# Kernel optimization log

Measured on AMD Instinct MI355X. Metric: run time of the kernel, lower is better.

## Reference

```python
import jax, jax.numpy as jnp
import numpy as np


def setup_inputs() -> dict:
    key = jax.random.key(0)
    k1, k2 = jax.random.split(key)
    B, N, M, D = 4, 8192, 8192, 3
    inp = jax.random.normal(k1, (B, N, D), dtype=jnp.float32)
    pnt = jax.random.normal(k2, (B, M, D), dtype=jnp.float32)
    return {"input": inp, "point": pnt}


def reference(input, point):
    # Per-query nearest-neighbor squared distance:
    # out[b, n] = min_m || input[b, n] - point[b, m] ||^2
    # Use ||a||^2 + ||b||^2 - 2 a.b to avoid materializing [B, N, M, D].
    sq_in = jnp.sum(input * input, axis=-1)          # [B, N]
    sq_pt = jnp.sum(point * point, axis=-1)          # [B, M]
    cross = jnp.einsum('bnd,bmd->bnm', input, point) # [B, N, M]
    d2 = sq_in[:, :, None] + sq_pt[:, None, :] - 2.0 * cross
    d2 = jnp.maximum(d2, 0.0)  # numerical guard
    return jnp.min(d2, axis=-1)  # [B, N]
```

## Files before the change

kernel.cpp:

```cpp
#include <hip/hip_runtime.h>
#include <hip/hip_bf16.h>

constexpr int B = 4;
constexpr int N = 8192;
constexpr int M = 8192;

constexpr int QPW     = 64;
constexpr int WAVES   = 4;
constexpr int QB      = QPW * WAVES;
constexpr int QTILES  = N / QB;
constexpr int PCHUNKS = 16;
constexpr int CHUNK   = M / PCHUNKS;
constexpr int PTILES  = CHUNK / 32;

typedef __bf16 bf16x8 __attribute__((ext_vector_type(8)));
typedef float  f32x16 __attribute__((ext_vector_type(16)));

union FragU { uint4 u; bf16x8 b; };

__device__ __host__ inline unsigned f2bf(float x) {
    unsigned u = __float_as_uint(x);
    return (u + 0x7FFFu + ((u >> 16) & 1u)) >> 16;
}
__device__ inline float bf2f(unsigned b) { return __uint_as_float(b << 16); }
__device__ inline unsigned pk(unsigned lo, unsigned hi) { return lo | (hi << 16); }


__global__ __launch_bounds__(256) void prep_kernel(const float* __restrict__ point,
                                                   uint4* __restrict__ wtab,
                                                   unsigned int* __restrict__ out) {
    int i = blockIdx.x * 256 + threadIdx.x;
    if (i >= B * M) return;
    const float p0 = point[3 * i + 0];
    const float p1 = point[3 * i + 1];
    const float p2 = point[3 * i + 2];
    const float v0 = -2.0f * p0, v1 = -2.0f * p1, v2 = -2.0f * p2;
    const unsigned h0 = f2bf(v0), l0 = f2bf(v0 - bf2f(h0));
    const unsigned h1 = f2bf(v1), l1 = f2bf(v1 - bf2f(h1));
    const unsigned h2 = f2bf(v2), l2 = f2bf(v2 - bf2f(h2));
    const float s = fmaf(p0, p0, fmaf(p1, p1, p2 * p2));
    const unsigned sh = f2bf(s), sl = f2bf(s - bf2f(sh));
    uint4 f0, f1;
    f0.x = pk(h0, h0); f0.y = pk(l0, l0); f0.z = pk(h1, h1); f0.w = pk(l1, l1);
    f1.x = pk(h2, h2); f1.y = pk(l2, l2); f1.z = pk(sh, sl); f1.w = 0;
    wtab[2 * i + 0] = f0;
    wtab[2 * i + 1] = f1;
    out[i] = 0x7F7F7F7Fu;
}

__device__ inline FragU make_bfrag(const float* __restrict__ input,
                                   int b, int q, int h, float& sq_a) {
    const float* a = input + ((size_t)b * N + q) * 3;
    const float a0 = a[0], a1 = a[1], a2 = a[2];
    sq_a = fmaf(a0, a0, fmaf(a1, a1, a2 * a2));
    const unsigned ah0 = f2bf(a0), al0 = f2bf(a0 - bf2f(ah0));
    const unsigned ah1 = f2bf(a1), al1 = f2bf(a1 - bf2f(ah1));
    const unsigned ah2 = f2bf(a2), al2 = f2bf(a2 - bf2f(ah2));
    FragU bq;
    const unsigned dA = h ? pk(ah2, al2) : pk(ah0, al0);
    const unsigned dB = h ? 0x3F803F80u  : pk(ah1, al1);
    bq.u.x = dA;
    bq.u.y = dA;
    bq.u.z = dB;
    bq.u.w = h ? 0u : dB;
    return bq;
}

__global__ __launch_bounds__(256, 3) void main_kernel(const float* __restrict__ input,
                                                      const uint4* __restrict__ wtab,
                                                      unsigned int* __restrict__ out) {
    const int bid    = blockIdx.x;
    const int pchunk = bid % PCHUNKS;
    const int qtile  = (bid / PCHUNKS) % QTILES;
    const int b      = bid / (PCHUNKS * QTILES);
    const int tid    = threadIdx.x;
    const int wave   = tid >> 6;
    const int lane   = tid & 63;
    const int col    = lane & 31;
    const int h      = lane >> 5;

    const int q0 = qtile * QB + wave * QPW + col;
    const int q1 = q0 + 32;
    float sq_a0, sq_a1;
    const FragU b0 = make_bfrag(input, b, q0, h, sq_a0);
    const FragU b1 = make_bfrag(input, b, q1, h, sq_a1);

    const uint4* __restrict__ wp =
        wtab + ((size_t)b * M + (size_t)pchunk * CHUNK) * 2;

    f32x16 cz, rmin0, rmin1;
#pragma unroll
    for (int i = 0; i < 16; ++i) { cz[i] = 0.0f; rmin0[i] = 1e30f; rmin1[i] = 1e30f; }

    for (int t = 0; t < PTILES; t += 2) {
        FragU fa0, fa1;
        fa0.u = wp[((t * 32 + col) << 1) + h];
        fa1.u = wp[(((t + 1) * 32 + col) << 1) + h];
        f32x16 acc00 = __builtin_amdgcn_mfma_f32_32x32x16_bf16(fa0.b, b0.b, cz, 0, 0, 0);
        f32x16 acc01 = __builtin_amdgcn_mfma_f32_32x32x16_bf16(fa0.b, b1.b, cz, 0, 0, 0);
        f32x16 acc10 = __builtin_amdgcn_mfma_f32_32x32x16_bf16(fa1.b, b0.b, cz, 0, 0, 0);
        f32x16 acc11 = __builtin_amdgcn_mfma_f32_32x32x16_bf16(fa1.b, b1.b, cz, 0, 0, 0);
#pragma unroll
        for (int i = 0; i < 16; ++i) {
            rmin0[i] = fminf(rmin0[i], fminf(acc00[i], acc10[i]));
            rmin1[i] = fminf(rmin1[i], fminf(acc01[i], acc11[i]));
        }
    }

    float m0 = rmin0[0], m1 = rmin1[0];
#pragma unroll
    for (int i = 1; i < 16; ++i) { m0 = fminf(m0, rmin0[i]); m1 = fminf(m1, rmin1[i]); }
    m0 = fminf(m0, __shfl_xor(m0, 32, 64));
    m1 = fminf(m1, __shfl_xor(m1, 32, 64));

    if (lane < 32) {
        atomicMin(&out[(size_t)b * N + q0], __float_as_uint(fmaxf(m0 + sq_a0, 0.0f)));
        atomicMin(&out[(size_t)b * N + q1], __float_as_uint(fmaxf(m1 + sq_a1, 0.0f)));
    }
}

extern "C" void kernel_launch(void* const* d_in, const int* in_sizes, int n_in,
                              void* d_out, int out_size, void* d_ws, size_t ws_size,
                              hipStream_t stream) {
    const float* input = (const float*)d_in[0];
    const float* point = (const float*)d_in[1];
    unsigned int* out  = (unsigned int*)d_out;

    uint4* wtab = (uint4*)d_ws;

    const int prep_grid = (B * M + 255) / 256;
    const int main_grid = B * QTILES * PCHUNKS;

    prep_kernel<<<prep_grid, 256, 0, stream>>>(point, wtab, out);
    main_kernel<<<main_grid, 256, 0, stream>>>(input, wtab, out);
}
```

Before: 66.52 us.

## Fuse point packing into main kernel via shared-memory tile, memset output

Removes the separate prep kernel and its global workspace table. Each block now loads its chunk of raw points, packs them into bf16 hi/lo fragments in LDS, and has the MFMA loop read from LDS instead of global memory. Output initialisation moves to a hipMemsetAsync. The packing work is repeated once per query tile (QTILES times per chunk), and the LDS footprint is 16KB per block, which may limit occupancy.

```diff
diff --git a/kernel.cpp b/kernel.cpp
--- a/kernel.cpp
+++ b/kernel.cpp
@@ -18,7 +18,7 @@
 
 union FragU { uint4 u; bf16x8 b; };
 
-__device__ __host__ inline unsigned f2bf(float x) {
+__device__ inline unsigned f2bf(float x) {
     unsigned u = __float_as_uint(x);
     return (u + 0x7FFFu + ((u >> 16) & 1u)) >> 16;
 }
@@ -26,26 +26,16 @@
 __device__ inline unsigned pk(unsigned lo, unsigned hi) { return lo | (hi << 16); }
 
 
-__global__ __launch_bounds__(256) void prep_kernel(const float* __restrict__ point,
-                                                   uint4* __restrict__ wtab,
-                                                   unsigned int* __restrict__ out) {
-    int i = blockIdx.x * 256 + threadIdx.x;
-    if (i >= B * M) return;
-    const float p0 = point[3 * i + 0];
-    const float p1 = point[3 * i + 1];
-    const float p2 = point[3 * i + 2];
+__device__ inline void pack_point(float p0, float p1, float p2,
+                                  uint4& f0, uint4& f1) {
     const float v0 = -2.0f * p0, v1 = -2.0f * p1, v2 = -2.0f * p2;
     const unsigned h0 = f2bf(v0), l0 = f2bf(v0 - bf2f(h0));
     const unsigned h1 = f2bf(v1), l1 = f2bf(v1 - bf2f(h1));
     const unsigned h2 = f2bf(v2), l2 = f2bf(v2 - bf2f(h2));
     const float s = fmaf(p0, p0, fmaf(p1, p1, p2 * p2));
     const unsigned sh = f2bf(s), sl = f2bf(s - bf2f(sh));
-    uint4 f0, f1;
     f0.x = pk(h0, h0); f0.y = pk(l0, l0); f0.z = pk(h1, h1); f0.w = pk(l1, l1);
     f1.x = pk(h2, h2); f1.y = pk(l2, l2); f1.z = pk(sh, sl); f1.w = 0;
-    wtab[2 * i + 0] = f0;
-    wtab[2 * i + 1] = f1;
-    out[i] = 0x7F7F7F7Fu;
 }
 
 __device__ inline FragU make_bfrag(const float* __restrict__ input,
@@ -67,7 +57,7 @@
 }
 
 __global__ __launch_bounds__(256, 3) void main_kernel(const float* __restrict__ input,
-                                                      const uint4* __restrict__ wtab,
+                                                      const float* __restrict__ point,
                                                       unsigned int* __restrict__ out) {
     const int bid    = blockIdx.x;
     const int pchunk = bid % PCHUNKS;
@@ -79,14 +69,32 @@
     const int col    = lane & 31;
     const int h      = lane >> 5;
 
+    __shared__ uint4 tile[2][CHUNK];
+
+    {
+        const float* pp = point + ((size_t)b * M + (size_t)pchunk * CHUNK) * 3;
+        const float2* pp2 = (const float2*)(pp + 6 * tid);
+        const float2 u0 = pp2[0];
+        const float2 u1 = pp2[1];
+        const float2 u2 = pp2[2];
+        uint4 f0, f1;
+        pack_point(u0.x, u0.y, u1.x, f0, f1);
+        tile[0][2 * tid + 0] = f0;
+        tile[1][2 * tid + 0] = f1;
+        pack_point(u1.y, u2.x, u2.y, f0, f1);
+        tile[0][2 * tid + 1] = f0;
+        tile[1][2 * tid + 1] = f1;
+    }
+
     const int q0 = qtile * QB + wave * QPW + col;
     const int q1 = q0 + 32;
     float sq_a0, sq_a1;
     const FragU b0 = make_bfrag(input, b, q0, h, sq_a0);
     const FragU b1 = make_bfrag(input, b, q1, h, sq_a1);
 
-    const uint4* __restrict__ wp =
-        wtab + ((size_t)b * M + (size_t)pchunk * CHUNK) * 2;
+    __syncthreads();
+
+    const uint4* __restrict__ th = &tile[h][0];
 
     f32x16 cz, rmin0, rmin1;
 #pragma unroll
@@ -94,8 +102,8 @@
 
     for (int t = 0; t < PTILES; t += 2) {
         FragU fa0, fa1;
-        fa0.u = wp[((t * 32 + col) << 1) + h];
-        fa1.u = wp[(((t + 1) * 32 + col) << 1) + h];
+        fa0.u = th[t * 32 + col];
+        fa1.u = th[(t + 1) * 32 + col];
         f32x16 acc00 = __builtin_amdgcn_mfma_f32_32x32x16_bf16(fa0.b, b0.b, cz, 0, 0, 0);
         f32x16 acc01 = __builtin_amdgcn_mfma_f32_32x32x16_bf16(fa0.b, b1.b, cz, 0, 0, 0);
         f32x16 acc10 = __builtin_amdgcn_mfma_f32_32x32x16_bf16(fa1.b, b0.b, cz, 0, 0, 0);
@@ -126,11 +134,8 @@
     const float* point = (const float*)d_in[1];
     unsigned int* out  = (unsigned int*)d_out;
 
-    uint4* wtab = (uint4*)d_ws;
+    (void)hipMemsetAsync(d_out, 0x7F, (size_t)out_size * sizeof(float), stream);
 
-    const int prep_grid = (B * M + 255) / 256;
     const int main_grid = B * QTILES * PCHUNKS;
-
-    prep_kernel<<<prep_grid, 256, 0, stream>>>(point, wtab, out);
-    main_kernel<<<main_grid, 256, 0, stream>>>(input, wtab, out);
+    main_kernel<<<main_grid, 256, 0, stream>>>(input, point, out);
 }
```

Result: slower. 73.41 us (+10.4%).
